# Performance work log

Measured on AMD Instinct MI355X. Metric: run time of the kernel, lower is better.

## Reference

```python
import jax, jax.numpy as jnp
import numpy as np
from jax import lax

ORDER = 6
WN = 0.5 / 50.0          # highpass_cutoff / (orig_fs/2)
UP, DOWN = 16, 25        # 64/100 reduced by gcd 4 (scipy resample_poly)
HALF_LEN = 10 * DOWN     # scipy kaiser half length = 10*max_rate
NTAPS = 2 * HALF_LEN + 1
PADLEN = 21              # sosfiltfilt default: 3*(2*n_sections+1), 3 biquads
CHANNELS = np.array([126, 125, 48, 112, 67, 93, 10, 61, 39, 108])
D_MODEL = 16
LN_EPS = 1e-5


def _butter_hp_sos(order, wn):
    # scipy.signal.butter(order, wn, btype='high', output='sos') in pure numpy
    fs = 2.0
    warped = 2.0 * fs * np.tan(np.pi * wn / fs)
    m = np.arange(-order + 1, order, 2)
    p = -np.exp(1j * np.pi * m / (2 * order))     # analog LP prototype poles
    k = np.real(1.0 / np.prod(-p))                # lp2hp gain (no zeros)
    p = warped / p                                # lp2hp poles; zeros at s=0
    z = np.zeros(order)
    fs2 = 2.0 * fs                                # bilinear, fs=2
    k = k * np.real(np.prod(fs2 - z) / np.prod(fs2 - p))
    z = (fs2 + z) / (fs2 - z)                     # digital zeros, all +1
    p = (fs2 + p) / (fs2 - p)
    pp = p[np.imag(p) > 0]
    pp = pp[np.argsort(-np.abs(np.abs(pp) - 1.0))]  # closest to unit circle last
    sos = []
    for i, pi in enumerate(pp):
        b = np.array([1.0, -2.0, 1.0]) * (k if i == 0 else 1.0)
        a = np.array([1.0, -2.0 * pi.real, np.abs(pi) ** 2])
        sos.append(np.concatenate([b, a]))
    return np.array(sos)


def _sosfilt_zi(sos):
    # scipy.signal.sosfilt_zi: steady-state of step response per section
    n = sos.shape[0]
    zi = np.zeros((n, 2))
    scale = 1.0
    for s in range(n):
        b0, b1, b2, _, a1, a2 = sos[s]
        A = np.array([[1.0 + a1, -1.0], [a2, 1.0]])
        B = np.array([b1 - a1 * b0, b2 - a2 * b0])
        zi[s] = scale * np.linalg.solve(A, B)
        scale *= (b0 + b1 + b2) / (1.0 + a1 + a2)
    return zi


SOS = _butter_hp_sos(ORDER, WN)
ZI = _sosfilt_zi(SOS)


def _resample_fir():
    # scipy firwin(2*half_len+1, 1/max_rate, window=('kaiser',5.0)) * up
    fc = 1.0 / DOWN
    m = np.arange(NTAPS) - (NTAPS - 1) / 2.0
    h = fc * np.sinc(fc * m) * np.kaiser(NTAPS, 5.0)
    h /= h.sum()
    return h * UP


H_BASE = _resample_fir()


def _pos_encoding(max_len, d):
    pos = np.arange(max_len)[:, None].astype(np.float64)
    div = np.exp(np.arange(0, d, 2) * (-np.log(10000.0) / d))
    pe = np.zeros((max_len, d))
    pe[:, 0::2] = np.sin(pos * div)
    pe[:, 1::2] = np.cos(pos * div)
    return pe.astype(np.float32)


PE = _pos_encoding(3840, D_MODEL)


def _sosfilt(x, zi):
    # x: (N,T), zi: (N,3,2). Cascade of biquads, transposed direct form II.
    sos = jnp.asarray(SOS, x.dtype)
    nsec = SOS.shape[0]

    def step(z, xt):
        v = xt
        zs = []
        for s in range(nsec):  # fixed tiny cascade, unrolled inside scan
            b0, b1, b2, a1, a2 = sos[s, 0], sos[s, 1], sos[s, 2], sos[s, 4], sos[s, 5]
            y = b0 * v + z[s][0]
            zs.append((b1 * v - a1 * y + z[s][1], b2 * v - a2 * y))
            v = y
        return tuple(zs), v

    z0 = tuple((zi[:, s, 0], zi[:, s, 1]) for s in range(nsec))
    _, y = lax.scan(step, z0, x.T)
    return y.T


def _sosfiltfilt(x):
    # scipy.signal.sosfiltfilt with default odd padding, padlen=21
    zi = jnp.asarray(ZI, x.dtype)
    front = 2.0 * x[:, :1] - x[:, PADLEN:0:-1]
    back = 2.0 * x[:, -1:] - x[:, -2:-PADLEN - 2:-1]
    ext = jnp.concatenate([front, x, back], axis=1)
    y = _sosfilt(ext, zi[None] * ext[:, 0, None, None])
    y = y[:, ::-1]
    y = _sosfilt(y, zi[None] * y[:, 0, None, None])
    return y[:, ::-1][:, PADLEN:-PADLEN]


def _resample_poly(x):
    # scipy.signal.resample_poly(x, 64, 100): upfirdn via dilated conv
    T = x.shape[-1]
    n_out = (T * UP) // DOWN + int((T * UP) % DOWN != 0)
    n_pre_pad = DOWN - HALF_LEN % DOWN
    n_pre_remove = (HALF_LEN + n_pre_pad) // DOWN

    def outlen(lh):
        return (((T - 1) * UP + lh) - 1) // DOWN + 1

    n_post = 0
    while outlen(NTAPS + n_pre_pad + n_post) < n_out + n_pre_remove:
        n_post += 1
    h = np.concatenate([np.zeros(n_pre_pad), H_BASE, np.zeros(n_post)])
    L = h.size
    rhs = jnp.asarray(h[::-1].copy(), x.dtype).reshape(1, 1, L)
    y = lax.conv_general_dilated(x[:, None, :], rhs, window_strides=(DOWN,),
                                 padding=[(L - 1, L - 1)], lhs_dilation=(UP,),
                                 dimension_numbers=('NCH', 'OIH', 'NCH'))
    return y[:, 0, n_pre_remove:n_pre_remove + n_out]


def _ln(x, g, b):
    mu = x.mean(-1, keepdims=True)
    var = ((x - mu) ** 2).mean(-1, keepdims=True)
    return (x - mu) * lax.rsqrt(var + LN_EPS) * g + b


def setup_inputs() -> dict:
    key = jax.random.key(0)
    ks = jax.random.split(key, 20)
    f32 = jnp.float32
    d = {
        'x': jax.random.normal(ks[0], (64, 128, 2000), f32),
        'conv_w': jax.random.normal(ks[1], (16, 10, 3), f32) * 0.15,
        'conv_b': jnp.zeros((16,), f32),
        'ln0_g': jnp.ones((16,), f32), 'ln0_b': jnp.zeros((16,), f32),
        'wqkv': jax.random.normal(ks[2], (48, 16), f32) * 0.125,
        'bqkv': jnp.zeros((48,), f32),
        'wo': jax.random.normal(ks[3], (16, 16), f32) * 0.25,
        'bo': jnp.zeros((16,), f32),
        'w1': jax.random.normal(ks[4], (32, 16), f32) * 0.2,
        'b1': jnp.zeros((32,), f32),
        'w2': jax.random.normal(ks[5], (16, 32), f32) * 0.2,
        'b2': jnp.zeros((16,), f32),
        'ln1_g': jnp.ones((16,), f32), 'ln1_b': jnp.zeros((16,), f32),
        'ln2_g': jnp.ones((16,), f32), 'ln2_b': jnp.zeros((16,), f32),
        'wfc': jax.random.normal(ks[6], (1, 16), f32) * 0.3,
        'bfc': jnp.zeros((1,), f32),
    }
    return d


def reference(x, conv_w, conv_b, ln0_g, ln0_b, wqkv, bqkv, wo, bo,
              w1, b1, w2, b2, ln1_g, ln1_b, ln2_g, ln2_b, wfc, bfc):
    B = x.shape[0]
    # remove Cz (last channel) then gather interesting channels
    x = x[:, :-1, :][:, jnp.asarray(CHANNELS), :]        # (B,10,T)
    x = x - x.mean(axis=1, keepdims=True)                # CAR
    C, T = x.shape[1], x.shape[2]
    xf = _sosfiltfilt(x.reshape(B * C, T))               # zero-phase highpass
    xr = _resample_poly(xf)                              # 100 Hz -> 64 Hz
    x = xr.reshape(B, C, -1)
    x = jnp.tanh(x)                                      # artifact_scale = 1.0
    mean = x.mean(axis=2, keepdims=True)                 # zscore, unbiased std
    var = ((x - mean) ** 2).sum(axis=2, keepdims=True) / (x.shape[2] - 1)
    std = jnp.maximum(jnp.sqrt(var), 1e-6)
    x = (x - mean) / std
    # conv1d k=3 pad=1 (10 -> 16) + relu
    x = lax.conv_general_dilated(x, conv_w, (1,), [(1, 1)],
                                 dimension_numbers=('NCH', 'OIH', 'NCH'))
    x = jax.nn.relu(x + conv_b[None, :, None])
    x = x.transpose(0, 2, 1)                             # (B,S,16)
    x = _ln(x, ln0_g, ln0_b)
    x = x + jnp.asarray(PE[:x.shape[1]], x.dtype)[None]
    # TransformerEncoderLayer, post-norm, nhead=1, relu FFN (eval: no dropout)
    qkv = x @ wqkv.T + bqkv
    q, k, v = jnp.split(qkv, 3, axis=-1)
    att = jax.nn.softmax(jnp.einsum('bqd,bkd->bqk', q, k) * 0.25, axis=-1)
    a = jnp.einsum('bqk,bkd->bqd', att, v) @ wo.T + bo
    x = _ln(x + a, ln1_g, ln1_b)
    f = jax.nn.relu(x @ w1.T + b1) @ w2.T + b2
    x = _ln(x + f, ln2_g, ln2_b)
    pooled = x.mean(axis=1)                              # adaptive avg pool -> 1
    return pooled @ wfc.T + bfc                          # (B,1)
```

## Files before the change

kernel.cpp:

```cpp
#include <hip/hip_runtime.h>
#include <cmath>
#include <complex>
#include <algorithm>

#ifndef M_PI
#define M_PI 3.14159265358979323846
#endif

typedef _Float16 f16x8 __attribute__((ext_vector_type(8)));
typedef _Float16 f16x4 __attribute__((ext_vector_type(4)));
typedef float f32x4 __attribute__((ext_vector_type(4)));

struct FiltArg {
  double b0[3], b1[3], b2[3], a1[3], a2[3];
  double zi0[3], zi1[3];
  double A32[36];
};
struct CorArg { double CA[32 * 6]; };
struct FirArg { float h[526]; };

static void design_sos(FiltArg& sa) {
  const int order = 6;
  const double wn = 0.5 / 50.0;
  const double fs = 2.0;
  double warped = 2.0 * fs * std::tan(M_PI * wn / fs);
  std::complex<double> p[6];
  for (int i = 0; i < order; i++) {
    int m = -order + 1 + 2 * i;
    p[i] = -std::exp(std::complex<double>(0.0, M_PI * m / (2.0 * order)));
  }
  std::complex<double> prod1(1, 0);
  for (int i = 0; i < 6; i++) prod1 *= -p[i];
  double k = (1.0 / prod1).real();
  for (int i = 0; i < 6; i++) p[i] = warped / p[i];
  const double fs2 = 2.0 * fs;
  std::complex<double> num(1, 0), den(1, 0);
  for (int i = 0; i < 6; i++) { num *= fs2; den *= (fs2 - p[i]); }
  k *= (num / den).real();
  for (int i = 0; i < 6; i++) p[i] = (fs2 + p[i]) / (fs2 - p[i]);
  std::complex<double> pp[3]; int n = 0;
  for (int i = 0; i < 6; i++) if (p[i].imag() > 0) pp[n++] = p[i];
  std::stable_sort(pp, pp + 3,
    [](const std::complex<double>& A, const std::complex<double>& B) {
      return std::fabs(std::abs(A) - 1.0) > std::fabs(std::abs(B) - 1.0);
    });
  double sos[3][6];
  for (int s = 0; s < 3; s++) {
    double g = (s == 0) ? k : 1.0;
    sos[s][0] = g; sos[s][1] = -2.0 * g; sos[s][2] = g;
    sos[s][3] = 1.0; sos[s][4] = -2.0 * pp[s].real(); sos[s][5] = std::norm(pp[s]);
  }
  double scale = 1.0;
  for (int s = 0; s < 3; s++) {
    double b0 = sos[s][0], b1 = sos[s][1], b2 = sos[s][2];
    double a1 = sos[s][4], a2 = sos[s][5];
    double det = 1.0 + a1 + a2;
    double r0 = b1 - a1 * b0, r1 = b2 - a2 * b0;
    double z0 = (r0 + r1) / det;
    double z1 = ((1.0 + a1) * r1 - a2 * r0) / det;
    sa.b0[s] = b0; sa.b1[s] = b1; sa.b2[s] = b2; sa.a1[s] = a1; sa.a2[s] = a2;
    sa.zi0[s] = scale * z0; sa.zi1[s] = scale * z1;
    scale *= (b0 + b1 + b2) / (1.0 + a1 + a2);
  }
}

static double host_step(const FiltArg& c, double z[6], double v) {
  for (int s = 0; s < 3; s++) {
    double y = c.b0[s] * v + z[2 * s];
    z[2 * s]     = c.b1[s] * v - c.a1[s] * y + z[2 * s + 1];
    z[2 * s + 1] = c.b2[s] * v - c.a2[s] * y;
    v = y;
  }
  return v;
}

static void build_filt(FiltArg& c, CorArg& co) {
  design_sos(c);
  double A[36];
  for (int j = 0; j < 6; j++) {
    double z[6] = {0, 0, 0, 0, 0, 0};
    z[j] = 1.0;
    host_step(c, z, 0.0);
    for (int i = 0; i < 6; i++) A[i * 6 + j] = z[i];
  }
  double M[36], T[36];
  for (int i = 0; i < 36; i++) M[i] = A[i];
  for (int sq = 0; sq < 5; sq++) {
    for (int i = 0; i < 6; i++)
      for (int j = 0; j < 6; j++) {
        double s = 0.0;
        for (int kk = 0; kk < 6; kk++) s += M[i * 6 + kk] * M[kk * 6 + j];
        T[i * 6 + j] = s;
      }
    for (int i = 0; i < 36; i++) M[i] = T[i];
  }
  for (int i = 0; i < 36; i++) c.A32[i] = M[i];
  for (int j = 0; j < 6; j++) {
    double z[6] = {0, 0, 0, 0, 0, 0};
    z[j] = 1.0;
    for (int i = 0; i < 32; i++) co.CA[i * 6 + j] = host_step(c, z, 0.0);
  }
}

static double bessel_i0(double x) {
  double s = 1.0, t = 1.0;
  for (int k = 1; k < 64; k++) {
    double u = x / (2.0 * k);
    t *= u * u; s += t;
    if (t < 1e-18 * s) break;
  }
  return s;
}

static void design_fir(FirArg& fa) {
  double h[501];
  const double fc = 1.0 / 25.0;
  double denom = bessel_i0(5.0);
  double sum = 0.0;
  for (int nn = 0; nn < 501; nn++) {
    double m = nn - 250.0;
    double xx = fc * m;
    double snc = (nn == 250) ? 1.0 : std::sin(M_PI * xx) / (M_PI * xx);
    double r = (2.0 * nn) / 500.0 - 1.0;
    double w = bessel_i0(5.0 * std::sqrt(std::max(0.0, 1.0 - r * r))) / denom;
    h[nn] = fc * snc * w; sum += h[nn];
  }
  for (int nn = 0; nn < 25; nn++) fa.h[nn] = 0.0f;
  for (int nn = 0; nn < 501; nn++) fa.h[25 + nn] = (float)(h[nn] / sum * 16.0);
}

__device__ inline double waveReduceSum(double v) {
  #pragma unroll
  for (int off = 32; off > 0; off >>= 1) v += __shfl_down(v, off, 64);
  return v;
}

__global__ __launch_bounds__(256) void k_chansel_pe(const float* __restrict__ x,
                                                    float* __restrict__ xs,
                                                    float* __restrict__ pe,
                                                    float* __restrict__ out) {
  int gid = blockIdx.x;
  if (gid < 500) {
    int idx = gid * 256 + threadIdx.x;
    int b = idx / 2000, t = idx % 2000;
    const int ch[10] = {126, 125, 48, 112, 67, 93, 10, 61, 39, 108};
    const float* xb = x + (size_t)b * 128 * 2000;
    float v[10]; float s = 0.f;
    #pragma unroll
    for (int c = 0; c < 10; c++) { v[c] = xb[ch[c] * 2000 + t]; s += v[c]; }
    s *= 0.1f;
    #pragma unroll
    for (int c = 0; c < 10; c++) xs[((size_t)b * 10 + c) * 2000 + t] = v[c] - s;
  } else {
    int i = (gid - 500) * 256 + threadIdx.x;
    int t = i >> 4, d = i & 15, j = d >> 1;
    double div = exp(-((double)(2 * j)) * 0.5756462732485114);
    double a = (double)t * div;
    pe[i] = (float)((d & 1) ? cos(a) : sin(a));
    if (gid == 579 && threadIdx.x < 64) out[threadIdx.x] = 0.f;
  }
}

#define XR(t) xr[(t) + ((t) >> 5)]
#define YF(t) yf[(t) + ((t) >> 5)]
__global__ __launch_bounds__(64) void k_filtfilt(float* __restrict__ xs,
                                                 FiltArg c, CorArg co) {
  __shared__ float xr[2112];
  __shared__ double yf[2112];
  __shared__ double Fs[64][7];
  __shared__ double Zs[64][7];
  int r = blockIdx.x;
  int k = threadIdx.x;
  float* x = xs + (size_t)r * 2000;

  float x0f = x[0], xlf = x[1999];
  for (int t = k; t < 2048; t += 64) {
    float v;
    if (t < 21)        v = 2.f * x0f - x[21 - t];
    else if (t < 2021) v = x[t - 21];
    else if (t < 2042) v = 2.f * xlf - x[4019 - t];
    else               v = 0.f;
    XR(t) = v;
  }
  __syncthreads();

  double b0[3], b1[3], b2[3], a1[3], a2[3];
  #pragma unroll
  for (int s = 0; s < 3; s++) {
    b0[s] = c.b0[s]; b1[s] = c.b1[s]; b2[s] = c.b2[s];
    a1[s] = c.a1[s]; a2[s] = c.a2[s];
  }
  auto step = [&](double* z, double v) -> double {
    #pragma unroll
    for (int s = 0; s < 3; s++) {
      double y = b0[s] * v + z[2 * s];
      z[2 * s]     = b1[s] * v - a1[s] * y + z[2 * s + 1];
      z[2 * s + 1] = b2[s] * v - a2[s] * y;
      v = y;
    }
    return v;
  };
  double arow[6] = {0, 0, 0, 0, 0, 0};
  if (k < 6) {
    #pragma unroll
    for (int j = 0; j < 6; j++) arow[j] = c.A32[k * 6 + j];
  }
  int li = (k < 6) ? k : 0;
  auto scan = [&](double seed) {
    double zz = 0.0;
    if (k < 6) zz = ((k & 1) ? c.zi1[k >> 1] : c.zi0[k >> 1]) * seed;
    for (int kk = 0; kk < 64; kk++) {
      if (k < 6) Zs[kk][k] = zz;
      double f = Fs[kk][li];
      double nz = f;
      #pragma unroll
      for (int j = 0; j < 6; j++) nz += arow[j] * __shfl(zz, j, 64);
      zz = nz;
    }
  };

  int t0 = k * 32;
  double z[6], yreg[32];

  #pragma unroll
  for (int i = 0; i < 6; i++) z[i] = 0.0;
  for (int i = 0; i < 32; i++) yreg[i] = step(z, (double)XR(t0 + i));
  #pragma unroll
  for (int i = 0; i < 6; i++) Fs[k][i] = z[i];
  __syncthreads();
  scan((double)XR(0));
  __syncthreads();
  #pragma unroll
  for (int i = 0; i < 6; i++) z[i] = Zs[k][i];
  for (int i = 0; i < 32; i++) {
    double corr = 0.0;
    #pragma unroll
    for (int j = 0; j < 6; j++) corr += co.CA[i * 6 + j] * z[j];
    YF(t0 + i) = yreg[i] + corr;
  }
  __syncthreads();

  auto rin = [&](int j) -> double { return (j <= 2041) ? YF(2041 - j) : 0.0; };
  #pragma unroll
  for (int i = 0; i < 6; i++) z[i] = 0.0;
  for (int i = 0; i < 32; i++) yreg[i] = step(z, rin(t0 + i));
  #pragma unroll
  for (int i = 0; i < 6; i++) Fs[k][i] = z[i];
  __syncthreads();
  scan(YF(2041));
  __syncthreads();
  #pragma unroll
  for (int i = 0; i < 6; i++) z[i] = Zs[k][i];
  for (int i = 0; i < 32; i++) {
    int j = t0 + i;
    if (j >= 21 && j <= 2020) {
      double corr = 0.0;
      #pragma unroll
      for (int jj = 0; jj < 6; jj++) corr += co.CA[i * 6 + jj] * z[jj];
      x[2020 - j] = (float)(yreg[i] + corr);
    }
  }
}

__global__ __launch_bounds__(256) void k_resample_norm(const float* __restrict__ xf,
                                                       float* __restrict__ xn,
                                                       FirArg fa) {
  __shared__ float xl[2000];
  __shared__ float hl[526];
  int r = blockIdx.x;
  const float* x = xf + (size_t)r * 2000;
  for (int i = threadIdx.x; i < 2000; i += 256) xl[i] = x[i];
  for (int i = threadIdx.x; i < 526; i += 256) hl[i] = fa.h[i];
  __syncthreads();
  float vals[5];
  #pragma unroll
  for (int kk = 0; kk < 5; kk++) {
    int o = threadIdx.x + kk * 256;
    int P = 25 * (o + 11);
    int phase = P & 15;
    float acc = 0.f;
    for (int m = phase; m <= 525; m += 16) {
      int idx = (P - m) >> 4;
      if (idx >= 0 && idx < 2000) acc += hl[m] * xl[idx];
    }
    vals[kk] = tanhf(acc);
  }
  double s = 0.0, ss = 0.0;
  #pragma unroll
  for (int kk = 0; kk < 5; kk++) {
    s += (double)vals[kk]; ss += (double)vals[kk] * (double)vals[kk];
  }
  s = waveReduceSum(s); ss = waveReduceSum(ss);
  __shared__ double red[8];
  int wid = threadIdx.x >> 6, lane = threadIdx.x & 63;
  if (lane == 0) { red[wid] = s; red[4 + wid] = ss; }
  __syncthreads();
  double S = red[0] + red[1] + red[2] + red[3];
  double SS = red[4] + red[5] + red[6] + red[7];
  double mean = S / 1280.0;
  double var = (SS - 1280.0 * mean * mean) / 1279.0;
  double sd = fmax(sqrt(fmax(var, 0.0)), 1e-6);
  float fmean = (float)mean, finv = (float)(1.0 / sd);
  #pragma unroll
  for (int kk = 0; kk < 5; kk++)
    xn[(size_t)r * 1280 + threadIdx.x + kk * 256] = (vals[kk] - fmean) * finv;
}

__global__ __launch_bounds__(256) void k_conv_ln_pe_qkv(const float* __restrict__ xn,
    const float* __restrict__ cw, const float* __restrict__ cb,
    const float* __restrict__ g0, const float* __restrict__ bt0,
    const float* __restrict__ wqkv, const float* __restrict__ bqkv,
    const float* __restrict__ pe,
    float* __restrict__ x0,
    float* __restrict__ Q, float* __restrict__ K, float* __restrict__ V) {
  __shared__ float w[480], bias[16], gg[16], gb[16];
  __shared__ float wq[768], bq[48];
  for (int i = threadIdx.x; i < 480; i += 256) w[i] = cw[i];
  for (int i = threadIdx.x; i < 768; i += 256) wq[i] = wqkv[i];
  if (threadIdx.x < 16) {
    bias[threadIdx.x] = cb[threadIdx.x];
    gg[threadIdx.x] = g0[threadIdx.x];
    gb[threadIdx.x] = bt0[threadIdx.x];
  }
  if (threadIdx.x < 48) bq[threadIdx.x] = bqkv[threadIdx.x];
  __syncthreads();
  int idx = blockIdx.x * 256 + threadIdx.x;
  int b = idx / 1280, t = idx % 1280;
  const float* xb = xn + (size_t)b * 10 * 1280;
  float in[10][3];
  #pragma unroll
  for (int i = 0; i < 10; i++)
    #pragma unroll
    for (int k = 0; k < 3; k++) {
      int tt = t - 1 + k;
      in[i][k] = (tt >= 0 && tt < 1280) ? xb[i * 1280 + tt] : 0.f;
    }
  float o[16];
  #pragma unroll
  for (int oc = 0; oc < 16; oc++) {
    float a = bias[oc];
    #pragma unroll
    for (int i = 0; i < 10; i++)
      #pragma unroll
      for (int k = 0; k < 3; k++) a += in[i][k] * w[oc * 30 + i * 3 + k];
    o[oc] = fmaxf(a, 0.f);
  }
  float mu = 0.f;
  #pragma unroll
  for (int d = 0; d < 16; d++) mu += o[d];
  mu *= (1.f / 16.f);
  float var = 0.f;
  #pragma unroll
  for (int d = 0; d < 16; d++) { float dd = o[d] - mu; var += dd * dd; }
  var *= (1.f / 16.f);
  float inv = 1.f / sqrtf(var + 1e-5f);
  float xv[16];
  float* outp = x0 + (size_t)idx * 16;
  const float* pep = pe + t * 16;
  #pragma unroll
  for (int d = 0; d < 16; d++) {
    xv[d] = (o[d] - mu) * inv * gg[d] + gb[d] + pep[d];
    outp[d] = xv[d];
  }
  float* qp = Q + (size_t)idx * 16;
  float* kp = K + (size_t)idx * 16;
  float* vp = V + (size_t)idx * 16;
  #pragma unroll
  for (int j = 0; j < 16; j++) {
    float a = bq[j];
    #pragma unroll
    for (int d = 0; d < 16; d++) a += xv[d] * wq[j * 16 + d];
    qp[j] = a;
  }
  #pragma unroll
  for (int j = 0; j < 16; j++) {
    float a = bq[16 + j];
    #pragma unroll
    for (int d = 0; d < 16; d++) a += xv[d] * wq[(16 + j) * 16 + d];
    kp[j] = a;
  }
  #pragma unroll
  for (int j = 0; j < 16; j++) {
    float a = bq[32 + j];
    #pragma unroll
    for (int d = 0; d < 16; d++) a += xv[d] * wq[(32 + j) * 16 + d];
    vp[j] = a;
  }
}

#define ATT_SHIFT 12.0f
__global__ __launch_bounds__(256) void k_attn_mfma(const float* __restrict__ Q,
    const float* __restrict__ K, const float* __restrict__ V,
    float* __restrict__ A) {
  __shared__ __align__(16) _Float16 Ks[64 * 40];
  __shared__ __align__(16) _Float16 Vt[16 * 72];
  __shared__ __align__(16) _Float16 Pld[4][16 * 40];
  int tid = threadIdx.x;
  int b  = blockIdx.x / 20;
  int rg = blockIdx.x % 20;
  int wv = tid >> 6;
  int lane = tid & 63;
  int col = lane & 15;
  int quad = lane >> 4;
  size_t base = (size_t)b * 1280;
  int row0 = rg * 64 + wv * 16;

  f16x8 qf;
  #pragma unroll
  for (int j = 0; j < 8; j++) qf[j] = (_Float16)0.f;
  if (quad < 2) {
    const float* qp = Q + (base + row0 + col) * 16 + quad * 8;
    #pragma unroll
    for (int j = 0; j < 8; j++) qf[j] = (_Float16)(0.25f * qp[j]);
  }
  f32x4 oacc = {0.f, 0.f, 0.f, 0.f};
  float lacc = 0.f;

  for (int s = 0; s < 20; s++) {
    __syncthreads();
    {
      int key = tid >> 2, part = tid & 3;
      const float* kp = K + (base + s * 64 + key) * 16 + part * 4;
      f16x4 hk, hz;
      #pragma unroll
      for (int j = 0; j < 4; j++) { hk[j] = (_Float16)kp[j]; hz[j] = (_Float16)0.f; }
      *(f16x4*)&Ks[key * 40 + part * 4] = hk;
      *(f16x4*)&Ks[key * 40 + 16 + part * 4] = hz;
      const float* vp = V + (base + s * 64 + key) * 16 + part * 4;
      #pragma unroll
      for (int j = 0; j < 4; j++) Vt[(part * 4 + j) * 72 + key] = (_Float16)vp[j];
    }
    __syncthreads();
    #pragma unroll
    for (int c = 0; c < 2; c++) {
      #pragma unroll
      for (int t = 0; t < 2; t++) {
        int keyoff = c * 32 + t * 16;
        f16x8 af = *(f16x8*)&Ks[(keyoff + col) * 40 + quad * 8];
        f32x4 sf = {0.f, 0.f, 0.f, 0.f};
        sf = __builtin_amdgcn_mfma_f32_16x16x32_f16(af, qf, sf, 0, 0, 0);
        f16x4 ph;
        float psum = 0.f;
        #pragma unroll
        for (int r = 0; r < 4; r++) {
          float p = __expf(sf[r] - ATT_SHIFT);
          psum += p;
          ph[r] = (_Float16)p;
        }
        lacc += psum;
        *(f16x4*)&Pld[wv][col * 40 + t * 16 + quad * 4] = ph;
      }
      __syncthreads();
      f16x8 pf = *(f16x8*)&Pld[wv][col * 40 + quad * 8];
      f16x8 vf = *(f16x8*)&Vt[col * 72 + c * 32 + quad * 8];
      oacc = __builtin_amdgcn_mfma_f32_16x16x32_f16(pf, vf, oacc, 0, 0, 0);
      __syncthreads();
    }
  }
  lacc += __shfl_xor(lacc, 16, 64);
  lacc += __shfl_xor(lacc, 32, 64);
  #pragma unroll
  for (int r = 0; r < 4; r++) {
    float lr = __shfl(lacc, quad * 4 + r, 64);
    A[(base + row0 + quad * 4 + r) * 16 + col] = oacc[r] / lr;
  }
}

__global__ __launch_bounds__(256) void k_combine_pool(
    const float* __restrict__ A, const float* __restrict__ x0,
    const float* __restrict__ wo, const float* __restrict__ bo,
    const float* __restrict__ w1, const float* __restrict__ b1,
    const float* __restrict__ w2, const float* __restrict__ b2,
    const float* __restrict__ g1, const float* __restrict__ bb1,
    const float* __restrict__ g2, const float* __restrict__ bb2,
    const float* __restrict__ wfc, const float* __restrict__ bfc,
    float* __restrict__ out) {
  __shared__ float swo[256], sw1[512], sw2[512];
  __shared__ float sbo[16], sb1[32], sb2[16], sg1[16], sbb1[16], sg2[16], sbb2[16];
  __shared__ float swf[16];
  int tid = threadIdx.x;
  swo[tid] = wo[tid];
  for (int i = tid; i < 512; i += 256) { sw1[i] = w1[i]; sw2[i] = w2[i]; }
  if (tid < 16) {
    sbo[tid] = bo[tid]; sb2[tid] = b2[tid];
    sg1[tid] = g1[tid]; sbb1[tid] = bb1[tid];
    sg2[tid] = g2[tid]; sbb2[tid] = bb2[tid];
    swf[tid] = wfc[tid];
  }
  if (tid < 32) sb1[tid] = b1[tid];
  __syncthreads();

  int idx = blockIdx.x * 256 + tid;
  int bb = blockIdx.x / 5;
  const float* pa = A + (size_t)idx * 16;
  float a[16];
  #pragma unroll
  for (int d = 0; d < 16; d++) a[d] = pa[d];
  float h[16];
  const float* xr = x0 + (size_t)idx * 16;
  #pragma unroll
  for (int d = 0; d < 16; d++) {
    float o = sbo[d];
    #pragma unroll
    for (int e = 0; e < 16; e++) o += a[e] * swo[d * 16 + e];
    h[d] = xr[d] + o;
  }
  float mu = 0.f;
  #pragma unroll
  for (int d = 0; d < 16; d++) mu += h[d];
  mu *= (1.f / 16.f);
  float var = 0.f;
  #pragma unroll
  for (int d = 0; d < 16; d++) { float dd = h[d] - mu; var += dd * dd; }
  var *= (1.f / 16.f);
  float inv = 1.f / sqrtf(var + 1e-5f);
  float x1[16];
  #pragma unroll
  for (int d = 0; d < 16; d++) x1[d] = (h[d] - mu) * inv * sg1[d] + sbb1[d];
  float t1[32];
  #pragma unroll
  for (int j = 0; j < 32; j++) {
    float u = sb1[j];
    #pragma unroll
    for (int d = 0; d < 16; d++) u += x1[d] * sw1[j * 16 + d];
    t1[j] = fmaxf(u, 0.f);
  }
  float h2[16];
  #pragma unroll
  for (int d = 0; d < 16; d++) {
    float u = sb2[d];
    #pragma unroll
    for (int j = 0; j < 32; j++) u += t1[j] * sw2[d * 32 + j];
    h2[d] = x1[d] + u;
  }
  mu = 0.f;
  #pragma unroll
  for (int d = 0; d < 16; d++) mu += h2[d];
  mu *= (1.f / 16.f);
  var = 0.f;
  #pragma unroll
  for (int d = 0; d < 16; d++) { float dd = h2[d] - mu; var += dd * dd; }
  var *= (1.f / 16.f);
  inv = 1.f / sqrtf(var + 1e-5f);
  float pv = 0.f;
  #pragma unroll
  for (int d = 0; d < 16; d++)
    pv += ((h2[d] - mu) * inv * sg2[d] + sbb2[d]) * swf[d];
  double part = waveReduceSum((double)pv);
  __shared__ double red[4];
  int wid = tid >> 6, lane = tid & 63;
  if (lane == 0) red[wid] = part;
  __syncthreads();
  if (tid == 0) {
    double S = red[0] + red[1] + red[2] + red[3];
    float add = (float)(S / 1280.0);
    if (blockIdx.x % 5 == 0) add += bfc[0];
    atomicAdd(&out[bb], add);
  }
}

extern "C" void kernel_launch(void* const* d_in, const int* in_sizes, int n_in,
                              void* d_out, int out_size, void* d_ws, size_t ws_size,
                              hipStream_t stream) {
  const float* x    = (const float*)d_in[0];
  const float* cw   = (const float*)d_in[1];
  const float* cb   = (const float*)d_in[2];
  const float* g0   = (const float*)d_in[3];
  const float* bt0  = (const float*)d_in[4];
  const float* wqkv = (const float*)d_in[5];
  const float* bqkv = (const float*)d_in[6];
  const float* wo   = (const float*)d_in[7];
  const float* bo   = (const float*)d_in[8];
  const float* w1   = (const float*)d_in[9];
  const float* b1   = (const float*)d_in[10];
  const float* w2   = (const float*)d_in[11];
  const float* b2   = (const float*)d_in[12];
  const float* g1   = (const float*)d_in[13];
  const float* bb1  = (const float*)d_in[14];
  const float* g2   = (const float*)d_in[15];
  const float* bb2  = (const float*)d_in[16];
  const float* wfc  = (const float*)d_in[17];
  const float* bfc  = (const float*)d_in[18];
  float* out = (float*)d_out;

  float* ws = (float*)d_ws;
  float* xs = ws;
  float* y1 = xs + 1280000;
  float* xn = y1 + 1306880;
  float* x0 = xn + 819200;
  float* Q  = x0 + 1310720;
  float* Kb = Q  + 1310720;
  float* Vb = Kb + 1310720;
  float* pe = Vb + 1310720;
  float* Abuf = ws;

  FiltArg fc; CorArg co; FirArg fa;
  build_filt(fc, co);
  design_fir(fa);

  k_chansel_pe<<<580, 256, 0, stream>>>(x, xs, pe, out);
  k_filtfilt<<<640, 64, 0, stream>>>(xs, fc, co);
  k_resample_norm<<<640, 256, 0, stream>>>(xs, xn, fa);
  k_conv_ln_pe_qkv<<<320, 256, 0, stream>>>(xn, cw, cb, g0, bt0, wqkv, bqkv,
                                            pe, x0, Q, Kb, Vb);
  k_attn_mfma<<<1280, 256, 0, stream>>>(Q, Kb, Vb, Abuf);
  k_combine_pool<<<320, 256, 0, stream>>>(Abuf, x0, wo, bo, w1, b1, w2, b2,
                                          g1, bb1, g2, bb2, wfc, bfc, out);
}
```

Before: 250.7 us.

## Fuse filtfilt with polyphase resample and compute FIR taps on device

Merges the zero-phase IIR filter kernel and the resample/tanh/zscore kernel so the filtered row stays in shared memory instead of being written to and re-read from global memory. The resample phase now runs with 64 threads per block, each computing 20 outputs, and the normalization reduction becomes a single-wave shuffle. The Kaiser FIR design moves from host to an extra block of the channel-select kernel, writing taps to a workspace buffer and removing the large by-value kernel argument. The trade-off is less parallelism for the resample arithmetic per row.

```diff
diff --git a/kernel.cpp b/kernel.cpp
--- a/kernel.cpp
+++ b/kernel.cpp
@@ -17,7 +17,6 @@
   double A32[36];
 };
 struct CorArg { double CA[32 * 6]; };
-struct FirArg { float h[526]; };
 
 static void design_sos(FiltArg& sa) {
   const int order = 6;
@@ -102,7 +101,13 @@
   }
 }
 
-static double bessel_i0(double x) {
+__device__ inline double waveReduceSum(double v) {
+  #pragma unroll
+  for (int off = 32; off > 0; off >>= 1) v += __shfl_down(v, off, 64);
+  return v;
+}
+
+__device__ inline double dbessel_i0(double x) {
   double s = 1.0, t = 1.0;
   for (int k = 1; k < 64; k++) {
     double u = x / (2.0 * k);
@@ -112,36 +117,15 @@
   return s;
 }
 
-static void design_fir(FirArg& fa) {
-  double h[501];
-  const double fc = 1.0 / 25.0;
-  double denom = bessel_i0(5.0);
-  double sum = 0.0;
-  for (int nn = 0; nn < 501; nn++) {
-    double m = nn - 250.0;
-    double xx = fc * m;
-    double snc = (nn == 250) ? 1.0 : std::sin(M_PI * xx) / (M_PI * xx);
-    double r = (2.0 * nn) / 500.0 - 1.0;
-    double w = bessel_i0(5.0 * std::sqrt(std::max(0.0, 1.0 - r * r))) / denom;
-    h[nn] = fc * snc * w; sum += h[nn];
-  }
-  for (int nn = 0; nn < 25; nn++) fa.h[nn] = 0.0f;
-  for (int nn = 0; nn < 501; nn++) fa.h[25 + nn] = (float)(h[nn] / sum * 16.0);
-}
-
-__device__ inline double waveReduceSum(double v) {
-  #pragma unroll
-  for (int off = 32; off > 0; off >>= 1) v += __shfl_down(v, off, 64);
-  return v;
-}
-
 __global__ __launch_bounds__(256) void k_chansel_pe(const float* __restrict__ x,
                                                     float* __restrict__ xs,
                                                     float* __restrict__ pe,
+                                                    float* __restrict__ hbuf,
                                                     float* __restrict__ out) {
   int gid = blockIdx.x;
+  int tid = threadIdx.x;
   if (gid < 500) {
-    int idx = gid * 256 + threadIdx.x;
+    int idx = gid * 256 + tid;
     int b = idx / 2000, t = idx % 2000;
     const int ch[10] = {126, 125, 48, 112, 67, 93, 10, 61, 39, 108};
     const float* xb = x + (size_t)b * 128 * 2000;
@@ -151,28 +135,55 @@
     s *= 0.1f;
     #pragma unroll
     for (int c = 0; c < 10; c++) xs[((size_t)b * 10 + c) * 2000 + t] = v[c] - s;
-  } else {
-    int i = (gid - 500) * 256 + threadIdx.x;
+  } else if (gid < 580) {
+    int i = (gid - 500) * 256 + tid;
     int t = i >> 4, d = i & 15, j = d >> 1;
     double div = exp(-((double)(2 * j)) * 0.5756462732485114);
     double a = (double)t * div;
     pe[i] = (float)((d & 1) ? cos(a) : sin(a));
-    if (gid == 579 && threadIdx.x < 64) out[threadIdx.x] = 0.f;
+    if (gid == 579 && tid < 64) out[tid] = 0.f;
+  } else {
+    __shared__ double hd[501];
+    __shared__ double red[4];
+    const double fc = 1.0 / 25.0;
+    double denom = dbessel_i0(5.0);
+    for (int nn = tid; nn < 501; nn += 256) {
+      double m = nn - 250.0;
+      double xx = fc * m;
+      double snc = (nn == 250) ? 1.0 : sin(M_PI * xx) / (M_PI * xx);
+      double r = (2.0 * nn) / 500.0 - 1.0;
+      double w = dbessel_i0(5.0 * sqrt(fmax(0.0, 1.0 - r * r))) / denom;
+      hd[nn] = fc * snc * w;
+    }
+    __syncthreads();
+    double s = 0.0;
+    for (int nn = tid; nn < 501; nn += 256) s += hd[nn];
+    s = waveReduceSum(s);
+    int wid = tid >> 6, lane = tid & 63;
+    if (lane == 0) red[wid] = s;
+    __syncthreads();
+    double sum = red[0] + red[1] + red[2] + red[3];
+    for (int i = tid; i < 526; i += 256)
+      hbuf[i] = (i < 25) ? 0.f : (float)(hd[i - 25] / sum * 16.0);
   }
 }
 
 #define XR(t) xr[(t) + ((t) >> 5)]
 #define YF(t) yf[(t) + ((t) >> 5)]
-__global__ __launch_bounds__(64) void k_filtfilt(float* __restrict__ xs,
-                                                 FiltArg c, CorArg co) {
+__global__ __launch_bounds__(64) void k_filt_resample(const float* __restrict__ xs,
+                                                      float* __restrict__ xn,
+                                                      const float* __restrict__ hglob,
+                                                      FiltArg c, CorArg co) {
   __shared__ float xr[2112];
   __shared__ double yf[2112];
   __shared__ double Fs[64][7];
   __shared__ double Zs[64][7];
+  __shared__ float hl[526];
   int r = blockIdx.x;
   int k = threadIdx.x;
-  float* x = xs + (size_t)r * 2000;
-
+  const float* x = xs + (size_t)r * 2000;
+
+  for (int i = k; i < 526; i += 64) hl[i] = hglob[i];
   float x0f = x[0], xlf = x[1999];
   for (int t = k; t < 2048; t += 64) {
     float v;
@@ -257,53 +268,39 @@
       double corr = 0.0;
       #pragma unroll
       for (int jj = 0; jj < 6; jj++) corr += co.CA[i * 6 + jj] * z[jj];
-      x[2020 - j] = (float)(yreg[i] + corr);
-    }
-  }
-}
-
-__global__ __launch_bounds__(256) void k_resample_norm(const float* __restrict__ xf,
-                                                       float* __restrict__ xn,
-                                                       FirArg fa) {
-  __shared__ float xl[2000];
-  __shared__ float hl[526];
-  int r = blockIdx.x;
-  const float* x = xf + (size_t)r * 2000;
-  for (int i = threadIdx.x; i < 2000; i += 256) xl[i] = x[i];
-  for (int i = threadIdx.x; i < 526; i += 256) hl[i] = fa.h[i];
-  __syncthreads();
-  float vals[5];
-  #pragma unroll
-  for (int kk = 0; kk < 5; kk++) {
-    int o = threadIdx.x + kk * 256;
+      XR(2020 - j) = (float)(yreg[i] + corr);
+    }
+  }
+  __syncthreads();
+
+  float vals[20];
+  #pragma unroll 4
+  for (int j = 0; j < 20; j++) {
+    int o = k + j * 64;
     int P = 25 * (o + 11);
     int phase = P & 15;
     float acc = 0.f;
     for (int m = phase; m <= 525; m += 16) {
       int idx = (P - m) >> 4;
-      if (idx >= 0 && idx < 2000) acc += hl[m] * xl[idx];
-    }
-    vals[kk] = tanhf(acc);
+      if (idx >= 0 && idx < 2000) acc += hl[m] * XR(idx);
+    }
+    vals[j] = tanhf(acc);
   }
   double s = 0.0, ss = 0.0;
   #pragma unroll
-  for (int kk = 0; kk < 5; kk++) {
-    s += (double)vals[kk]; ss += (double)vals[kk] * (double)vals[kk];
+  for (int j = 0; j < 20; j++) {
+    s += (double)vals[j]; ss += (double)vals[j] * (double)vals[j];
   }
   s = waveReduceSum(s); ss = waveReduceSum(ss);
-  __shared__ double red[8];
-  int wid = threadIdx.x >> 6, lane = threadIdx.x & 63;
-  if (lane == 0) { red[wid] = s; red[4 + wid] = ss; }
-  __syncthreads();
-  double S = red[0] + red[1] + red[2] + red[3];
-  double SS = red[4] + red[5] + red[6] + red[7];
-  double mean = S / 1280.0;
-  double var = (SS - 1280.0 * mean * mean) / 1279.0;
+  s = __shfl(s, 0, 64); ss = __shfl(ss, 0, 64);
+  double mean = s / 1280.0;
+  double var = (ss - 1280.0 * mean * mean) / 1279.0;
   double sd = fmax(sqrt(fmax(var, 0.0)), 1e-6);
   float fmean = (float)mean, finv = (float)(1.0 / sd);
-  #pragma unroll
-  for (int kk = 0; kk < 5; kk++)
-    xn[(size_t)r * 1280 + threadIdx.x + kk * 256] = (vals[kk] - fmean) * finv;
+  float* xo = xn + (size_t)r * 1280;
+  #pragma unroll
+  for (int j = 0; j < 20; j++)
+    xo[k + j * 64] = (vals[j] - fmean) * finv;
 }
 
 __global__ __launch_bounds__(256) void k_conv_ln_pe_qkv(const float* __restrict__ xn,
@@ -592,15 +589,14 @@
   float* Kb = Q  + 1310720;
   float* Vb = Kb + 1310720;
   float* pe = Vb + 1310720;
+  float* hbuf = pe + 20480;
   float* Abuf = ws;
 
-  FiltArg fc; CorArg co; FirArg fa;
+  FiltArg fc; CorArg co;
   build_filt(fc, co);
-  design_fir(fa);
-
-  k_chansel_pe<<<580, 256, 0, stream>>>(x, xs, pe, out);
-  k_filtfilt<<<640, 64, 0, stream>>>(xs, fc, co);
-  k_resample_norm<<<640, 256, 0, stream>>>(xs, xn, fa);
+
+  k_chansel_pe<<<581, 256, 0, stream>>>(x, xs, pe, hbuf, out);
+  k_filt_resample<<<640, 64, 0, stream>>>(xs, xn, hbuf, fc, co);
   k_conv_ln_pe_qkv<<<320, 256, 0, stream>>>(xn, cw, cb, g0, bt0, wqkv, bqkv,
                                             pe, x0, Q, Kb, Vb);
   k_attn_mfma<<<1280, 256, 0, stream>>>(Q, Kb, Vb, Abuf);
```

After: 296.8 us. +18.4%, slower.
